# Performance work log

Hardware: AMD Instinct MI355X
Metric: run time of the kernel (lower is better)

The kernel has to match this reference:

```python
import jax, jax.numpy as jnp
import numpy as np
import math

T = 0.28
EPS = 1e-06
D_MODEL = 1024
N_HEADS = 16
D_K = D_MODEL // N_HEADS


def compute_radius(t, epsilon):
    raw = math.sqrt(4.0 * t * math.log(1.0 / epsilon))
    return max(int(math.ceil(raw * 2.0)), 1)

RADIUS = compute_radius(T, EPS)  # = 8 for t=0.28, eps=1e-6
WIN = RADIUS + 1                 # causal band window: j in [i-RADIUS, i]


def setup_inputs() -> dict:
    key = jax.random.key(0)
    ks = jax.random.split(key, 5)
    B, S = 2, 4096
    x = jax.random.normal(ks[0], (B, S, D_MODEL), dtype=jnp.float32)
    scale = 1.0 / math.sqrt(D_MODEL)
    Wq = jax.random.normal(ks[1], (D_MODEL, D_MODEL), dtype=jnp.float32) * scale
    Wk = jax.random.normal(ks[2], (D_MODEL, D_MODEL), dtype=jnp.float32) * scale
    Wv = jax.random.normal(ks[3], (D_MODEL, D_MODEL), dtype=jnp.float32) * scale
    Wo = jax.random.normal(ks[4], (D_MODEL, D_MODEL), dtype=jnp.float32) * scale
    return {"x": x, "Wq": Wq, "Wk": Wk, "Wv": Wv, "Wo": Wo}


def reference(x, Wq, Wk, Wv, Wo):
    B, S, _ = x.shape

    def split_heads(h):  # (B,S,D) -> (B,H,S,dk)
        return h.reshape(B, S, N_HEADS, D_K).transpose(0, 2, 1, 3)

    q = split_heads(x @ Wq)
    k = split_heads(x @ Wk)
    v = split_heads(x @ Wv)

    # Banded causal attention: token i attends to j in [i-RADIUS, i].
    # This equals the full masked softmax in the torch reference because
    # all out-of-band / non-causal entries are -inf there.
    pos = jnp.arange(S)
    idx = pos[:, None] + jnp.arange(-RADIUS, 1)[None, :]
    valid = idx >= 0                                       # left boundary
    idx_c = jnp.clip(idx, 0, S - 1)

    k_win = k[:, :, idx_c, :]
    v_win = v[:, :, idx_c, :]

    scores = jnp.einsum('bhsd,bhswd->bhsw', q, k_win) / (2.0 * T)
    scores = jnp.where(valid[None, None, :, :], scores, -jnp.inf)
    wts = jax.nn.softmax(scores, axis=-1)
    wts = jnp.nan_to_num(wts, nan=0.0)  # diagonal always valid, but keep parity

    attn = jnp.einsum('bhsw,bhswd->bhsd', wts, v_win)      # (B,H,S,dk)
    attn = attn.transpose(0, 2, 1, 3).reshape(B, S, D_MODEL)
    return attn @ Wo
```

## Files before the change

kernel.cpp:

```cpp
#include <hip/hip_runtime.h>
#include <stdint.h>

constexpr int S_LEN = 4096;
constexpr int DM    = 1024;
constexpr int RAD   = 8;
constexpr float INV2T = 1.7857142857142858f;

constexpr int BM = 128, BN = 128, BK = 64;

typedef _Float16 h8v __attribute__((ext_vector_type(8)));
typedef float f32x4  __attribute__((ext_vector_type(4)));

static __device__ __forceinline__ void gl_lds16(const void* gp, void* lp) {
  auto g = (const __attribute__((address_space(1))) void*)(uintptr_t)gp;
  auto l = (__attribute__((address_space(3))) void*)(uint32_t)(uintptr_t)lp;
  __builtin_amdgcn_global_load_lds(g, l, 16, 0, 0);
}

__global__ __launch_bounds__(256) void sda_prep_kernel(
    const float* __restrict__ X, _Float16* __restrict__ XH,
    const float* __restrict__ W0, const float* __restrict__ W1,
    const float* __restrict__ W2, const float* __restrict__ W3,
    _Float16* __restrict__ T0, _Float16* __restrict__ T1,
    _Float16* __restrict__ T2, _Float16* __restrict__ T3) {
  __shared__ float t[32][33];
  int z = blockIdx.z;
  int tx = threadIdx.x, ty = threadIdx.y;
  if (z < 4) {
    const float* W = z == 0 ? W0 : (z == 1 ? W1 : (z == 2 ? W2 : W3));
    _Float16*    T = z == 0 ? T0 : (z == 1 ? T1 : (z == 2 ? T2 : T3));
    int n0 = blockIdx.x * 32, k0 = blockIdx.y * 32;
#pragma unroll
    for (int i = 0; i < 4; ++i)
      t[ty + 8 * i][tx] = W[(size_t)(k0 + ty + 8 * i) * DM + n0 + tx];
    __syncthreads();
#pragma unroll
    for (int i = 0; i < 4; ++i)
      T[(size_t)(n0 + ty + 8 * i) * DM + k0 + tx] = (_Float16)t[tx][ty + 8 * i];
  } else {
    int blk = (z - 4) * 1024 + blockIdx.y * 32 + blockIdx.x;
    int i = blk * 256 + ty * 32 + tx;
    const float4* x4 = (const float4*)X;
    float4 a = x4[2 * i], b = x4[2 * i + 1];
    float f[8] = {a.x, a.y, a.z, a.w, b.x, b.y, b.z, b.w};
    union { _Float16 h[8]; uint4 v; } o;
#pragma unroll
    for (int j = 0; j < 8; ++j) o.h[j] = (_Float16)f[j];
    ((uint4*)XH)[i] = o.v;
  }
}

__global__ __launch_bounds__(256) void sda_gemm_swz_kernel(
    const _Float16* __restrict__ A, const _Float16* __restrict__ Bt,
    _Float16* __restrict__ C0, _Float16* __restrict__ C1,
    _Float16* __restrict__ C2) {
  constexpr int Kd = DM;
  __shared__ __align__(16) _Float16 As[BM * BK];
  __shared__ __align__(16) _Float16 Bs[BN * BK];

  int blk = blockIdx.x;
  int xcd = blk & 7, slot = blk >> 3;
  int xt = slot >> 3, ys = slot & 7;
  int yt = (xcd << 3) | ys;
  int m0 = yt * BM, n0 = xt * BN;

  int tid = threadIdx.x, wid = tid >> 6, lane = tid & 63;
  int srow = lane >> 3;
  int sgk = ((lane & 7) ^ (srow & 7)) * 8;
  int wm = (wid >> 1) * 64, wn = (wid & 1) * 64;
  int fm = lane & 15, fc = lane >> 4;

  f32x4 acc[4][4] = {};

  for (int kt = 0; kt < Kd / BK; ++kt) {
    if (kt) __syncthreads();
    int kk = kt * BK;
    int r0 = wid * 32;
#pragma unroll
    for (int i = 0; i < 4; ++i) {
      gl_lds16(A  + (size_t)(m0 + r0 + i * 8 + srow) * Kd + kk + sgk, &As[(r0 + i * 8) * BK]);
      gl_lds16(Bt + (size_t)(n0 + r0 + i * 8 + srow) * Kd + kk + sgk, &Bs[(r0 + i * 8) * BK]);
    }
    __syncthreads();

#pragma unroll
    for (int ks = 0; ks < 2; ++ks) {
      h8v af[4], bfr[4];
#pragma unroll
      for (int i = 0; i < 4; ++i) {
        int row = wm + i * 16 + fm;
        af[i] = *(const h8v*)&As[row * BK + (((ks * 4 + fc) ^ (row & 7)) * 8)];
      }
#pragma unroll
      for (int j = 0; j < 4; ++j) {
        int row = wn + j * 16 + fm;
        bfr[j] = *(const h8v*)&Bs[row * BK + (((ks * 4 + fc) ^ (row & 7)) * 8)];
      }
#pragma unroll
      for (int i = 0; i < 4; ++i)
#pragma unroll
        for (int j = 0; j < 4; ++j)
          acc[i][j] = __builtin_amdgcn_mfma_f32_16x16x32_f16(af[i], bfr[j], acc[i][j], 0, 0, 0);
    }
  }

  int which = n0 >> 10, nc = n0 & 1023;
  _Float16* Cv = which == 0 ? C0 : (which == 1 ? C1 : C2);

  int rr = (lane >> 4) * 4, cc = lane & 15;
#pragma unroll
  for (int i = 0; i < 4; ++i)
#pragma unroll
    for (int j = 0; j < 4; ++j) {
      size_t base = (size_t)(m0 + wm + i * 16 + rr) * DM + (nc + wn + j * 16 + cc);
#pragma unroll
      for (int r = 0; r < 4; ++r)
        Cv[base + (size_t)r * DM] = (_Float16)acc[i][j][r];
    }
}

__global__ __launch_bounds__(256) void sda_gemm_wo_kernel(
    const _Float16* __restrict__ A, const _Float16* __restrict__ Bt,
    float* __restrict__ C) {
  constexpr int Kd = DM, BN2 = 64;
  __shared__ __align__(16) _Float16 As[BM * BK];
  __shared__ __align__(16) _Float16 Bs[BN2 * BK];

  int blk = blockIdx.x;
  int xcd = blk & 7, slot = blk >> 3;
  int xt = slot >> 3, ys = slot & 7;
  int yt = (xcd << 3) | ys;
  int m0 = yt * BM, n0 = xt * BN2;

  int tid = threadIdx.x, wid = tid >> 6, lane = tid & 63;
  int srow = lane >> 3;
  int sgk = ((lane & 7) ^ (srow & 7)) * 8;
  int wm = (wid >> 1) * 64, wn = (wid & 1) * 32;
  int fm = lane & 15, fc = lane >> 4;

  f32x4 acc[4][2] = {};

  for (int kt = 0; kt < Kd / BK; ++kt) {
    if (kt) __syncthreads();
    int kk = kt * BK;
#pragma unroll
    for (int i = 0; i < 4; ++i)
      gl_lds16(A + (size_t)(m0 + wid * 32 + i * 8 + srow) * Kd + kk + sgk,
               &As[(wid * 32 + i * 8) * BK]);
#pragma unroll
    for (int i = 0; i < 2; ++i)
      gl_lds16(Bt + (size_t)(n0 + wid * 16 + i * 8 + srow) * Kd + kk + sgk,
               &Bs[(wid * 16 + i * 8) * BK]);
    __syncthreads();

#pragma unroll
    for (int ks = 0; ks < 2; ++ks) {
      h8v af[4], bfr[2];
#pragma unroll
      for (int i = 0; i < 4; ++i) {
        int row = wm + i * 16 + fm;
        af[i] = *(const h8v*)&As[row * BK + (((ks * 4 + fc) ^ (row & 7)) * 8)];
      }
#pragma unroll
      for (int j = 0; j < 2; ++j) {
        int row = wn + j * 16 + fm;
        bfr[j] = *(const h8v*)&Bs[row * BK + (((ks * 4 + fc) ^ (row & 7)) * 8)];
      }
#pragma unroll
      for (int i = 0; i < 4; ++i)
#pragma unroll
        for (int j = 0; j < 2; ++j)
          acc[i][j] = __builtin_amdgcn_mfma_f32_16x16x32_f16(af[i], bfr[j], acc[i][j], 0, 0, 0);
    }
  }

  int rr = (lane >> 4) * 4, cc = lane & 15;
#pragma unroll
  for (int i = 0; i < 4; ++i)
#pragma unroll
    for (int j = 0; j < 2; ++j) {
      size_t base = (size_t)(m0 + wm + i * 16 + rr) * DM + (n0 + wn + j * 16 + cc);
#pragma unroll
      for (int r = 0; r < 4; ++r)
        C[base + (size_t)r * DM] = acc[i][j][r];
    }
}

__global__ __launch_bounds__(256) void sda_attn_kernel(
    const _Float16* __restrict__ Q, const _Float16* __restrict__ K,
    const _Float16* __restrict__ V, _Float16* __restrict__ O) {
  constexpr int VTS = 104;
  __shared__ __align__(16) _Float16 ks[80 * 64];
  __shared__ __align__(16) _Float16 vst[64 * VTS];
  __shared__ __align__(16) float    scb[4 * 16 * 33];
  __shared__ __align__(16) _Float16 wts[64 * 96];

  int bh = blockIdx.y, b = bh >> 4, h = bh & 15;
  int s0 = blockIdx.x * 64;
  int tid = threadIdx.x;
  size_t headoff = (size_t)b * S_LEN * DM + h * 64;

  int wid = tid >> 6, lane = tid & 63;
  int fm = lane & 15, fkg = (lane >> 4) * 8;
  int rr = (lane >> 4) * 4, cc = lane & 15;

  const _Float16* qrow = Q + headoff + (size_t)(s0 + wid * 16 + fm) * DM;
  h8v aq0 = *(const h8v*)(qrow + fkg);
  h8v aq1 = *(const h8v*)(qrow + 32 + fkg);

  for (int idx = tid; idx < 72 * 8; idx += 256) {
    int row = idx >> 3, ch = (idx & 7) * 8;
    int pos = s0 - RAD + row;
    uint4 kv = make_uint4(0, 0, 0, 0);
    if (pos >= 0) kv = *(const uint4*)(K + headoff + (size_t)pos * DM + ch);
    *(uint4*)&ks[row * 64 + ch] = kv;
  }
  for (int idx = tid; idx < 72 * 8; idx += 256) {
    int row = idx % 72, chb = (idx / 72) * 8;
    int pos = s0 - RAD + row;
    uint4 vv = make_uint4(0, 0, 0, 0);
    if (pos >= 0) vv = *(const uint4*)(V + headoff + (size_t)pos * DM + chb);
    union { uint4 v; _Float16 hh[8]; } u; u.v = vv;
#pragma unroll
    for (int d = 0; d < 8; ++d) vst[(chb + d) * VTS + row] = u.hh[d];
  }
  if (tid < 64)
    *(uint4*)&ks[(72 + (tid >> 3)) * 64 + (tid & 7) * 8] = make_uint4(0, 0, 0, 0);
  for (int idx = tid; idx < 64 * 6; idx += 256) {
    int dim = idx / 6, p = idx % 6;
    *(uint2*)&vst[dim * VTS + 72 + p * 4] = make_uint2(0, 0);
  }
  for (int idx = tid; idx < 768; idx += 256)
    ((uint4*)wts)[idx] = make_uint4(0, 0, 0, 0);
  __syncthreads();

  {
    f32x4 accs[2] = {};
#pragma unroll
    for (int ti = 0; ti < 2; ++ti) {
      int t = wid + ti;
      h8v bk0 = *(const h8v*)&ks[(t * 16 + fm) * 64 + fkg];
      h8v bk1 = *(const h8v*)&ks[(t * 16 + fm) * 64 + 32 + fkg];
      accs[ti] = __builtin_amdgcn_mfma_f32_16x16x32_f16(aq0, bk0, accs[ti], 0, 0, 0);
      accs[ti] = __builtin_amdgcn_mfma_f32_16x16x32_f16(aq1, bk1, accs[ti], 0, 0, 0);
    }
#pragma unroll
    for (int ti = 0; ti < 2; ++ti)
#pragma unroll
      for (int r = 0; r < 4; ++r)
        scb[wid * 528 + (rr + r) * 33 + ti * 16 + cc] = accs[ti][r];
  }
  __syncthreads();

  if (tid < 64) {
    int r = tid, s = s0 + r;
    const float* my = &scb[(r >> 4) * 528 + (r & 15) * 33 + (r & 15)];
    float e[9], mx = -1e30f;
#pragma unroll
    for (int j = 0; j < 9; ++j) {
      float p = my[j] * INV2T;
      e[j] = (s - RAD + j >= 0) ? p : -1e30f;
      mx = fmaxf(mx, e[j]);
    }
    float se = 0.f;
#pragma unroll
    for (int j = 0; j < 9; ++j) { e[j] = __expf(e[j] - mx); se += e[j]; }
    float inv = 1.f / se;
#pragma unroll
    for (int j = 0; j < 9; ++j)
      wts[r * 96 + r + j] = (_Float16)(e[j] * inv);
  }
  __syncthreads();

  f32x4 acco[4] = {};
#pragma unroll
  for (int step = 0; step < 3; ++step) {
    h8v aw = *(const h8v*)&wts[(wid * 16 + fm) * 96 + step * 32 + fkg];
    int kb = step * 32 + fkg;
#pragma unroll
    for (int t = 0; t < 4; ++t) {
      h8v bv = *(const h8v*)&vst[(t * 16 + fm) * VTS + kb];
      acco[t] = __builtin_amdgcn_mfma_f32_16x16x32_f16(aw, bv, acco[t], 0, 0, 0);
    }
  }
#pragma unroll
  for (int t = 0; t < 4; ++t)
#pragma unroll
    for (int r = 0; r < 4; ++r)
      O[headoff + (size_t)(s0 + wid * 16 + rr + r) * DM + t * 16 + cc] =
          (_Float16)acco[t][r];
}

extern "C" void kernel_launch(void* const* d_in, const int* in_sizes, int n_in,
                              void* d_out, int out_size, void* d_ws, size_t ws_size,
                              hipStream_t stream) {
  (void)in_sizes; (void)n_in; (void)out_size; (void)ws_size;
  const float* x  = (const float*)d_in[0];
  const float* Wq = (const float*)d_in[1];
  const float* Wk = (const float*)d_in[2];
  const float* Wv = (const float*)d_in[3];
  const float* Wo = (const float*)d_in[4];

  char* ws = (char*)d_ws;
  const size_t MB = 1ull << 20;
  _Float16* xh    = (_Float16*)(ws + 0);
  _Float16* WqkvT = (_Float16*)(ws + 16 * MB);
  _Float16* WoT   = (_Float16*)(ws + 22 * MB);
  _Float16* Qh    = (_Float16*)(ws + 24 * MB);
  _Float16* Kh    = (_Float16*)(ws + 40 * MB);
  _Float16* Vh    = (_Float16*)(ws + 56 * MB);
  _Float16* Ah    = (_Float16*)(ws + 72 * MB);

  sda_prep_kernel<<<dim3(32, 32, 8), dim3(32, 8), 0, stream>>>(
      x, xh, Wq, Wk, Wv, Wo,
      WqkvT, WqkvT + (size_t)DM * DM, WqkvT + 2ull * DM * DM, WoT);

  sda_gemm_swz_kernel<<<1536, 256, 0, stream>>>(xh, WqkvT, Qh, Kh, Vh);
  sda_attn_kernel<<<dim3(64, 32), 256, 0, stream>>>(Qh, Kh, Vh, Ah);
  sda_gemm_wo_kernel<<<1024, 256, 0, stream>>>(Ah, WoT, (float*)d_out);
}
```

Baseline: 189.9 us.

## Widen Wo GEMM tile and make attention per-wave without block barriers

The output-projection GEMM moves from 128x64 to 128x128 tiles, halving the grid to 512 blocks. This raises MFMA work per LDS load but lowers parallelism to roughly two blocks per CU. The attention kernel now gives each wave its own 16-query slice with private K/V/score/weight LDS buffers. That removes all __syncthreads and shrinks the P·V MFMA loop from three k-steps to one, at the cost of each wave reloading overlapping K/V rows.

```diff
diff --git a/kernel.cpp b/kernel.cpp
--- a/kernel.cpp
+++ b/kernel.cpp
@@ -50,7 +50,7 @@
   }
 }
 
-__global__ __launch_bounds__(256) void sda_gemm_swz_kernel(
+__global__ __launch_bounds__(256) void sda_gemm_qkv_kernel(
     const _Float16* __restrict__ A, const _Float16* __restrict__ Bt,
     _Float16* __restrict__ C0, _Float16* __restrict__ C1,
     _Float16* __restrict__ C2) {
@@ -122,54 +122,52 @@
 __global__ __launch_bounds__(256) void sda_gemm_wo_kernel(
     const _Float16* __restrict__ A, const _Float16* __restrict__ Bt,
     float* __restrict__ C) {
-  constexpr int Kd = DM, BN2 = 64;
+  constexpr int Kd = DM;
   __shared__ __align__(16) _Float16 As[BM * BK];
-  __shared__ __align__(16) _Float16 Bs[BN2 * BK];
+  __shared__ __align__(16) _Float16 Bs[BN * BK];
 
   int blk = blockIdx.x;
   int xcd = blk & 7, slot = blk >> 3;
   int xt = slot >> 3, ys = slot & 7;
   int yt = (xcd << 3) | ys;
-  int m0 = yt * BM, n0 = xt * BN2;
+  int m0 = yt * BM, n0 = xt * BN;
 
   int tid = threadIdx.x, wid = tid >> 6, lane = tid & 63;
   int srow = lane >> 3;
   int sgk = ((lane & 7) ^ (srow & 7)) * 8;
-  int wm = (wid >> 1) * 64, wn = (wid & 1) * 32;
+  int wm = (wid >> 1) * 64, wn = (wid & 1) * 64;
   int fm = lane & 15, fc = lane >> 4;
 
-  f32x4 acc[4][2] = {};
+  f32x4 acc[4][4] = {};
 
   for (int kt = 0; kt < Kd / BK; ++kt) {
     if (kt) __syncthreads();
     int kk = kt * BK;
-#pragma unroll
-    for (int i = 0; i < 4; ++i)
-      gl_lds16(A + (size_t)(m0 + wid * 32 + i * 8 + srow) * Kd + kk + sgk,
-               &As[(wid * 32 + i * 8) * BK]);
-#pragma unroll
-    for (int i = 0; i < 2; ++i)
-      gl_lds16(Bt + (size_t)(n0 + wid * 16 + i * 8 + srow) * Kd + kk + sgk,
-               &Bs[(wid * 16 + i * 8) * BK]);
+    int r0 = wid * 32;
+#pragma unroll
+    for (int i = 0; i < 4; ++i) {
+      gl_lds16(A  + (size_t)(m0 + r0 + i * 8 + srow) * Kd + kk + sgk, &As[(r0 + i * 8) * BK]);
+      gl_lds16(Bt + (size_t)(n0 + r0 + i * 8 + srow) * Kd + kk + sgk, &Bs[(r0 + i * 8) * BK]);
+    }
     __syncthreads();
 
 #pragma unroll
     for (int ks = 0; ks < 2; ++ks) {
-      h8v af[4], bfr[2];
+      h8v af[4], bfr[4];
 #pragma unroll
       for (int i = 0; i < 4; ++i) {
         int row = wm + i * 16 + fm;
         af[i] = *(const h8v*)&As[row * BK + (((ks * 4 + fc) ^ (row & 7)) * 8)];
       }
 #pragma unroll
-      for (int j = 0; j < 2; ++j) {
+      for (int j = 0; j < 4; ++j) {
         int row = wn + j * 16 + fm;
         bfr[j] = *(const h8v*)&Bs[row * BK + (((ks * 4 + fc) ^ (row & 7)) * 8)];
       }
 #pragma unroll
       for (int i = 0; i < 4; ++i)
 #pragma unroll
-        for (int j = 0; j < 2; ++j)
+        for (int j = 0; j < 4; ++j)
           acc[i][j] = __builtin_amdgcn_mfma_f32_16x16x32_f16(af[i], bfr[j], acc[i][j], 0, 0, 0);
     }
   }
@@ -178,7 +176,7 @@
 #pragma unroll
   for (int i = 0; i < 4; ++i)
 #pragma unroll
-    for (int j = 0; j < 2; ++j) {
+    for (int j = 0; j < 4; ++j) {
       size_t base = (size_t)(m0 + wm + i * 16 + rr) * DM + (n0 + wn + j * 16 + cc);
 #pragma unroll
       for (int r = 0; r < 4; ++r)
@@ -189,72 +187,77 @@
 __global__ __launch_bounds__(256) void sda_attn_kernel(
     const _Float16* __restrict__ Q, const _Float16* __restrict__ K,
     const _Float16* __restrict__ V, _Float16* __restrict__ O) {
-  constexpr int VTS = 104;
-  __shared__ __align__(16) _Float16 ks[80 * 64];
-  __shared__ __align__(16) _Float16 vst[64 * VTS];
-  __shared__ __align__(16) float    scb[4 * 16 * 33];
-  __shared__ __align__(16) _Float16 wts[64 * 96];
+  constexpr int KS  = 72;
+  constexpr int VTS = 40;
+  constexpr int WS  = 40;
+  __shared__ __align__(16) _Float16 kw[4][32 * KS];
+  __shared__ __align__(16) _Float16 vt[4][64 * VTS];
+  __shared__ __align__(16) float    sc[4][16 * 33];
+  __shared__ __align__(16) _Float16 wt[4][16 * WS];
 
   int bh = blockIdx.y, b = bh >> 4, h = bh & 15;
   int s0 = blockIdx.x * 64;
-  int tid = threadIdx.x;
+  int tid = threadIdx.x, wid = tid >> 6, lane = tid & 63;
   size_t headoff = (size_t)b * S_LEN * DM + h * 64;
 
-  int wid = tid >> 6, lane = tid & 63;
+  _Float16* kwp = kw[wid];
+  _Float16* vtp = vt[wid];
+  float*    scp = sc[wid];
+  _Float16* wtp = wt[wid];
+
+  int p0 = s0 + wid * 16 - RAD;
   int fm = lane & 15, fkg = (lane >> 4) * 8;
   int rr = (lane >> 4) * 4, cc = lane & 15;
+
+  {
+    uint4 z = make_uint4(0, 0, 0, 0);
+    ((uint4*)wtp)[lane] = z;
+    if (lane < 16) ((uint4*)wtp)[64 + lane] = z;
+    *(uint4*)&vtp[lane * VTS + 24] = z;
+  }
+
+#pragma unroll
+  for (int i = 0; i < 3; ++i) {
+    int item = i * 64 + lane;
+    int row = item >> 3, ch = (item & 7) * 8;
+    int pos = p0 + row;
+    uint4 kv = make_uint4(0, 0, 0, 0);
+    if (pos >= 0) kv = *(const uint4*)(K + headoff + (size_t)pos * DM + ch);
+    *(uint4*)&kwp[row * KS + ch] = kv;
+  }
+#pragma unroll
+  for (int i = 0; i < 3; ++i) {
+    int item = i * 64 + lane;
+    int row = item >> 3, chb = (item & 7) * 8;
+    int pos = p0 + row;
+    uint4 vv = make_uint4(0, 0, 0, 0);
+    if (pos >= 0) vv = *(const uint4*)(V + headoff + (size_t)pos * DM + chb);
+    union { uint4 v; _Float16 hh[8]; } u; u.v = vv;
+#pragma unroll
+    for (int d = 0; d < 8; ++d) vtp[(chb + d) * VTS + row] = u.hh[d];
+  }
 
   const _Float16* qrow = Q + headoff + (size_t)(s0 + wid * 16 + fm) * DM;
   h8v aq0 = *(const h8v*)(qrow + fkg);
   h8v aq1 = *(const h8v*)(qrow + 32 + fkg);
 
-  for (int idx = tid; idx < 72 * 8; idx += 256) {
-    int row = idx >> 3, ch = (idx & 7) * 8;
-    int pos = s0 - RAD + row;
-    uint4 kv = make_uint4(0, 0, 0, 0);
-    if (pos >= 0) kv = *(const uint4*)(K + headoff + (size_t)pos * DM + ch);
-    *(uint4*)&ks[row * 64 + ch] = kv;
-  }
-  for (int idx = tid; idx < 72 * 8; idx += 256) {
-    int row = idx % 72, chb = (idx / 72) * 8;
-    int pos = s0 - RAD + row;
-    uint4 vv = make_uint4(0, 0, 0, 0);
-    if (pos >= 0) vv = *(const uint4*)(V + headoff + (size_t)pos * DM + chb);
-    union { uint4 v; _Float16 hh[8]; } u; u.v = vv;
-#pragma unroll
-    for (int d = 0; d < 8; ++d) vst[(chb + d) * VTS + row] = u.hh[d];
-  }
-  if (tid < 64)
-    *(uint4*)&ks[(72 + (tid >> 3)) * 64 + (tid & 7) * 8] = make_uint4(0, 0, 0, 0);
-  for (int idx = tid; idx < 64 * 6; idx += 256) {
-    int dim = idx / 6, p = idx % 6;
-    *(uint2*)&vst[dim * VTS + 72 + p * 4] = make_uint2(0, 0);
-  }
-  for (int idx = tid; idx < 768; idx += 256)
-    ((uint4*)wts)[idx] = make_uint4(0, 0, 0, 0);
-  __syncthreads();
-
-  {
-    f32x4 accs[2] = {};
-#pragma unroll
-    for (int ti = 0; ti < 2; ++ti) {
-      int t = wid + ti;
-      h8v bk0 = *(const h8v*)&ks[(t * 16 + fm) * 64 + fkg];
-      h8v bk1 = *(const h8v*)&ks[(t * 16 + fm) * 64 + 32 + fkg];
-      accs[ti] = __builtin_amdgcn_mfma_f32_16x16x32_f16(aq0, bk0, accs[ti], 0, 0, 0);
-      accs[ti] = __builtin_amdgcn_mfma_f32_16x16x32_f16(aq1, bk1, accs[ti], 0, 0, 0);
-    }
-#pragma unroll
-    for (int ti = 0; ti < 2; ++ti)
-#pragma unroll
-      for (int r = 0; r < 4; ++r)
-        scb[wid * 528 + (rr + r) * 33 + ti * 16 + cc] = accs[ti][r];
-  }
-  __syncthreads();
-
-  if (tid < 64) {
-    int r = tid, s = s0 + r;
-    const float* my = &scb[(r >> 4) * 528 + (r & 15) * 33 + (r & 15)];
+  f32x4 accs[2] = {};
+#pragma unroll
+  for (int t = 0; t < 2; ++t) {
+    h8v bk0 = *(const h8v*)&kwp[(t * 16 + fm) * KS + fkg];
+    h8v bk1 = *(const h8v*)&kwp[(t * 16 + fm) * KS + 32 + fkg];
+    accs[t] = __builtin_amdgcn_mfma_f32_16x16x32_f16(aq0, bk0, accs[t], 0, 0, 0);
+    accs[t] = __builtin_amdgcn_mfma_f32_16x16x32_f16(aq1, bk1, accs[t], 0, 0, 0);
+  }
+#pragma unroll
+  for (int t = 0; t < 2; ++t)
+#pragma unroll
+    for (int r = 0; r < 4; ++r)
+      scp[(rr + r) * 33 + t * 16 + cc] = accs[t][r];
+
+  if (lane < 16) {
+    int r = lane, s = s0 + wid * 16 + r;
+    const float* my = &scp[r * 33 + r];
     float e[9], mx = -1e30f;
 #pragma unroll
     for (int j = 0; j < 9; ++j) {
@@ -268,20 +271,15 @@
     float inv = 1.f / se;
 #pragma unroll
     for (int j = 0; j < 9; ++j)
-      wts[r * 96 + r + j] = (_Float16)(e[j] * inv);
-  }
-  __syncthreads();
+      wtp[r * WS + r + j] = (_Float16)(e[j] * inv);
+  }
 
   f32x4 acco[4] = {};
-#pragma unroll
-  for (int step = 0; step < 3; ++step) {
-    h8v aw = *(const h8v*)&wts[(wid * 16 + fm) * 96 + step * 32 + fkg];
-    int kb = step * 32 + fkg;
-#pragma unroll
-    for (int t = 0; t < 4; ++t) {
-      h8v bv = *(const h8v*)&vst[(t * 16 + fm) * VTS + kb];
-      acco[t] = __builtin_amdgcn_mfma_f32_16x16x32_f16(aw, bv, acco[t], 0, 0, 0);
-    }
+  h8v aw = *(const h8v*)&wtp[fm * WS + fkg];
+#pragma unroll
+  for (int t = 0; t < 4; ++t) {
+    h8v bv = *(const h8v*)&vtp[(t * 16 + fm) * VTS + fkg];
+    acco[t] = __builtin_amdgcn_mfma_f32_16x16x32_f16(aw, bv, acco[t], 0, 0, 0);
   }
 #pragma unroll
   for (int t = 0; t < 4; ++t)
@@ -315,7 +313,7 @@
       x, xh, Wq, Wk, Wv, Wo,
       WqkvT, WqkvT + (size_t)DM * DM, WqkvT + 2ull * DM * DM, WoT);
 
-  sda_gemm_swz_kernel<<<1536, 256, 0, stream>>>(xh, WqkvT, Qh, Kh, Vh);
+  sda_gemm_qkv_kernel<<<1536, 256, 0, stream>>>(xh, WqkvT, Qh, Kh, Vh);
   sda_attn_kernel<<<dim3(64, 32), 256, 0, stream>>>(Qh, Kh, Vh, Ah);
-  sda_gemm_wo_kernel<<<1024, 256, 0, stream>>>(Ah, WoT, (float*)d_out);
-}
+  sda_gemm_wo_kernel<<<512, 256, 0, stream>>>(Ah, WoT, (float*)d_out);
+}
```

After: 185.0 us. 2.6% less time.
